# Optimization experiments

Measured on AMD Instinct MI355X. Metric: run time of the kernel, lower is better.

## Reference

```python
import jax, jax.numpy as jnp
import numpy as np
import math

DIM = 64
SCALE = math.sqrt(DIM)


def setup_inputs() -> dict:
    key = jax.random.key(0)
    k = jax.random.split(key, 6)
    B, N1, D, H, W = 4, 4096, DIM, 64, 64
    x = jax.random.normal(k[0], (B, N1, D), dtype=jnp.float32)
    y = jax.random.normal(k[1], (B, D, H, W), dtype=jnp.float32)
    # torch nn.Linear params: weight (out,in), bias (out,), uniform(-1/sqrt(in), 1/sqrt(in))
    bound = 1.0 / math.sqrt(D)
    w1 = jax.random.uniform(k[2], (D, D), jnp.float32, -bound, bound)
    b1 = jax.random.uniform(k[3], (D,), jnp.float32, -bound, bound)
    w2 = jax.random.uniform(k[4], (D, D), jnp.float32, -bound, bound)
    b2 = jax.random.uniform(k[5], (D,), jnp.float32, -bound, bound)
    return {"x": x, "y": y, "w1": w1, "b1": b1, "w2": w2, "b2": b2}


def reference(x, y, w1, b1, w2, b2):
    # x: (B, N1, D); y: (B, D, H, W)
    B, D, H, W = y.shape
    y_tok = jnp.transpose(y, (0, 2, 3, 1)).reshape(B, H * W, D)  # (B, N2, D)
    q1 = x @ w1.T + b1        # (B, N1, D)
    q2 = y_tok @ w2.T + b2    # (B, N2, D)
    attn = jnp.einsum('bnd,bmd->bnm', q1, q2) / SCALE  # (B, N1, N2)
    score = jax.nn.softmax(attn, axis=2)  # dropout is identity in eval
    # v1 = q1^T @ score, transposed -> (B, N2, D)
    v1 = jnp.einsum('bnd,bnm->bmd', q1, score)
    # v2 = q2^T @ score^T, transposed -> (B, N1, D)
    v2 = jnp.einsum('bmd,bnm->bnd', q2, score)
    v1_img = jnp.transpose(v1.reshape(B, H, W, D), (0, 3, 1, 2))  # (B, D, H, W)
    return (v2, v1_img)
```

## Files before the change

### kernel.cpp

```cpp
#include <hip/hip_runtime.h>
#include <hip/hip_bf16.h>


typedef __attribute__((ext_vector_type(8))) short s8v;
typedef __attribute__((ext_vector_type(4))) float f4v;
typedef unsigned short ushort_t;
typedef unsigned int uint_t;

constexpr int B = 4, N = 4096, D = 64, SPLIT = 8, MCH = N / SPLIT;
constexpr int CH = 64, NST = MCH / CH;
constexpr float C1 = 0.18033688011112042f;

#define MFMA(A, Bv, C) __builtin_amdgcn_mfma_f32_16x16x32_bf16(A, Bv, C, 0, 0, 0)

__device__ __forceinline__ ushort_t f2bf(float x) {
    __hip_bfloat16 h = __float2bfloat16(x);
    return *reinterpret_cast<ushort_t*>(&h);
}

__device__ __forceinline__ uint_t pk2(float lo, float hi) {
    __hip_bfloat162 h = __float22bfloat162_rn(make_float2(lo, hi));
    return *reinterpret_cast<uint_t*>(&h);
}

__device__ __forceinline__ float bf2f(ushort_t u) {
    return __uint_as_float(((uint_t)u) << 16);
}

__global__ __launch_bounds__(256) void k_proj_x(const float* __restrict__ x,
        const float* __restrict__ w, const float* __restrict__ bias,
        ushort_t* __restrict__ qb, ushort_t* __restrict__ qt) {
    __shared__ float Xs[64][68];
    __shared__ float Ws[64][68];
    __shared__ float Bs[64];
    const int b = blockIdx.y, n0 = blockIdx.x * 64, t = threadIdx.x;
    const float* xp = x + ((size_t)b * N + n0) * D;
    for (int j = t; j < 4096; j += 256) Xs[j >> 6][j & 63] = xp[j];
    for (int j = t; j < 4096; j += 256) Ws[j >> 6][j & 63] = w[j];
    if (t < 64) Bs[t] = bias[t];
    __syncthreads();
    const int d = t & 63, grp = t >> 6;
    float wr[64];
#pragma unroll
    for (int k4 = 0; k4 < 16; ++k4) {
        float4 v = *reinterpret_cast<const float4*>(&Ws[d][k4 * 4]);
        wr[4 * k4 + 0] = v.x; wr[4 * k4 + 1] = v.y;
        wr[4 * k4 + 2] = v.z; wr[4 * k4 + 3] = v.w;
    }
    for (int i = 0; i < 16; ++i) {
        const int r = grp * 16 + i;
        float acc = Bs[d];
#pragma unroll
        for (int k4 = 0; k4 < 16; ++k4) {
            float4 xv = *reinterpret_cast<const float4*>(&Xs[r][k4 * 4]);
            acc += xv.x * wr[4 * k4] + xv.y * wr[4 * k4 + 1] +
                   xv.z * wr[4 * k4 + 2] + xv.w * wr[4 * k4 + 3];
        }
        qb[((size_t)b * N + n0 + r) * D + d] = f2bf(acc);
        qt[((size_t)b * D + d) * N + n0 + r] = f2bf(acc);
    }
}

__global__ __launch_bounds__(256) void k_proj_y(const float* __restrict__ y,
        const float* __restrict__ w, const float* __restrict__ bias,
        ushort_t* __restrict__ qb, ushort_t* __restrict__ qt) {
    __shared__ float Ys[64][68];
    __shared__ float Ws[64][68];
    __shared__ float Bs[64];
    const int b = blockIdx.y, m0 = blockIdx.x * 64, t = threadIdx.x;
    const float* yp = y + (size_t)b * D * N;
    for (int j = t; j < 4096; j += 256) {
        int k = j >> 6, mm = j & 63;
        Ys[mm][k] = yp[(size_t)k * N + m0 + mm];
    }
    for (int j = t; j < 4096; j += 256) Ws[j >> 6][j & 63] = w[j];
    if (t < 64) Bs[t] = bias[t];
    __syncthreads();
    const int d = t & 63, grp = t >> 6;
    float wr[64];
#pragma unroll
    for (int k4 = 0; k4 < 16; ++k4) {
        float4 v = *reinterpret_cast<const float4*>(&Ws[d][k4 * 4]);
        wr[4 * k4 + 0] = v.x; wr[4 * k4 + 1] = v.y;
        wr[4 * k4 + 2] = v.z; wr[4 * k4 + 3] = v.w;
    }
    for (int i = 0; i < 16; ++i) {
        const int r = grp * 16 + i;
        float acc = Bs[d];
#pragma unroll
        for (int k4 = 0; k4 < 16; ++k4) {
            float4 xv = *reinterpret_cast<const float4*>(&Ys[r][k4 * 4]);
            acc += xv.x * wr[4 * k4] + xv.y * wr[4 * k4 + 1] +
                   xv.z * wr[4 * k4 + 2] + xv.w * wr[4 * k4 + 3];
        }
        qb[((size_t)b * N + m0 + r) * D + d] = f2bf(acc);
        qt[((size_t)b * D + d) * N + m0 + r] = f2bf(acc);
    }
}

template<bool WANT_SUM, bool OUT_DM>
__global__ __launch_bounds__(256, 4) void k_attn(
        const ushort_t* __restrict__ kbm,
        const ushort_t* __restrict__ qbm,
        const ushort_t* __restrict__ vtm,
        ushort_t* __restrict__ vout, float* __restrict__ ssump) {
    __shared__ ushort_t kbS[2][4096];
    __shared__ ushort_t ptS[4][2][512];
    const int b = blockIdx.z, sp = blockIdx.y;
    const int tid = threadIdx.x;
    const int w = tid >> 6, lane = tid & 63, g = lane >> 4, c = lane & 15;
    const int xs = (blockIdx.x & 7) * 4 + (blockIdx.x >> 3);
    const int wb = xs * 128 + w * 32;
    const int lo = sp * MCH;

    const int M = ((c >> 1) & 3) << 4;
    char* rowp0 = (char*)&ptS[w][0][0] + c * 64;
    char* rowp1 = (char*)&ptS[w][1][0] + c * 64;
    const int wo0 = (8 * g) ^ M, wo1 = (32 + 8 * g) ^ M;
    const int ro  = (16 * g) ^ M;

    const int swzc = (c & 7) << 4;

    s8v a[2][2];
#pragma unroll
    for (int rt = 0; rt < 2; ++rt) {
        const ushort_t* p = qbm + ((size_t)b * N + wb + rt * 16 + c) * D + 8 * g;
        a[rt][0] = *reinterpret_cast<const s8v*>(p);
        a[rt][1] = *reinterpret_cast<const s8v*>(p + 32);
    }

    const int s0 = tid * 16, s1 = s0 + 4096;
    const int p0 = s0 ^ (((s0 >> 7) & 7) << 4);
    const int p1 = s1 ^ (((s1 >> 7) & 7) << 4);
    const char* gkb = (const char*)(kbm + ((size_t)b * N + lo) * D);
    char* kb0 = (char*)&kbS[0][0];
    char* kb1 = (char*)&kbS[1][0];
    const ushort_t* vbase = vtm + ((size_t)b * D + c) * N + 8 * g;

    f4v accO[2][4] = {};
    float rs0 = 0.f, rs1 = 0.f;
    s8v kb[2][2], vt[4], pa0, pa1;

#define LDKB_LDS(KC, SUB)                                                     \
    {                                                                         \
        const char* _r0 = (KC) + (32 * (SUB) + c) * 128;                      \
        kb[0][0] = *reinterpret_cast<const s8v*>(_r0 + ((16 * g) ^ swzc));    \
        kb[0][1] = *reinterpret_cast<const s8v*>(_r0 + ((64 + 16 * g) ^ swzc)); \
        kb[1][0] = *reinterpret_cast<const s8v*>(_r0 + 2048 + ((16 * g) ^ swzc)); \
        kb[1][1] = *reinterpret_cast<const s8v*>(_r0 + 2048 + ((64 + 16 * g) ^ swzc)); \
    }
#define LDVT(P)                                                               \
    {                                                                         \
        _Pragma("unroll")                                                     \
        for (int dc = 0; dc < 4; ++dc)                                        \
            vt[dc] = *reinterpret_cast<const s8v*>(vbase + (size_t)dc * 16 * N + (P)); \
    }
#define QKEXP(PQ)                                                             \
    f4v PQ[2][2] = {};                                                        \
    __builtin_amdgcn_s_setprio(1);                                            \
    _Pragma("unroll")                                                         \
    for (int rt = 0; rt < 2; ++rt) {                                          \
        _Pragma("unroll")                                                     \
        for (int h = 0; h < 2; ++h) {                                         \
            PQ[rt][h] = MFMA(kb[h][0], a[rt][0], PQ[rt][h]);                  \
            PQ[rt][h] = MFMA(kb[h][1], a[rt][1], PQ[rt][h]);                  \
        }                                                                     \
    }                                                                         \
    __builtin_amdgcn_s_setprio(0);
#define PACKWRITE(PQ)                                                         \
    {                                                                         \
        _Pragma("unroll")                                                     \
        for (int rt = 0; rt < 2; ++rt) {                                      \
            char* rp = rt ? rowp1 : rowp0;                                    \
            float rsl = 0.f;                                                  \
            _Pragma("unroll")                                                 \
            for (int h = 0; h < 2; ++h) {                                     \
                float e0 = exp2f(PQ[rt][h][0] * C1);                          \
                float e1 = exp2f(PQ[rt][h][1] * C1);                          \
                float e2 = exp2f(PQ[rt][h][2] * C1);                          \
                float e3 = exp2f(PQ[rt][h][3] * C1);                          \
                if (WANT_SUM) rsl += (e0 + e1) + (e2 + e3);                   \
                uint2 pk = make_uint2(pk2(e0, e1), pk2(e2, e3));              \
                *reinterpret_cast<uint2*>(rp + (h ? wo1 : wo0)) = pk;         \
            }                                                                 \
            if (WANT_SUM) { if (rt) rs1 += rsl; else rs0 += rsl; }            \
        }                                                                     \
    }
#define PV()                                                                  \
    __builtin_amdgcn_s_setprio(1);                                            \
    _Pragma("unroll")                                                         \
    for (int dc = 0; dc < 4; ++dc) {                                          \
        accO[0][dc] = MFMA(pa0, vt[dc], accO[0][dc]);                         \
        accO[1][dc] = MFMA(pa1, vt[dc], accO[1][dc]);                         \
    }                                                                         \
    __builtin_amdgcn_s_setprio(0);
#define RDTILE()                                                              \
    pa0 = *reinterpret_cast<const s8v*>(rowp0 + ro);                          \
    pa1 = *reinterpret_cast<const s8v*>(rowp1 + ro);
#define SUBCHUNK(KC, SUB, M0)                                                 \
    {                                                                         \
        LDKB_LDS(KC, SUB)                                                     \
        QKEXP(pq)                                                             \
        PACKWRITE(pq)                                                         \
        LDVT(M0)                                                              \
        asm volatile("s_waitcnt lgkmcnt(0)" ::: "memory");                    \
        RDTILE()                                                              \
        PV()                                                                  \
    }

    {
        uint4 t0 = *reinterpret_cast<const uint4*>(gkb + s0);
        uint4 t1 = *reinterpret_cast<const uint4*>(gkb + s1);
        *reinterpret_cast<uint4*>(kb0 + p0) = t0;
        *reinterpret_cast<uint4*>(kb0 + p1) = t1;
    }
    __syncthreads();

    for (int i = 0; i < NST; ++i) {
        char* kcur = (i & 1) ? kb1 : kb0;
        char* knxt = (i & 1) ? kb0 : kb1;
        const char* gn = gkb + (((i + 1) & (NST - 1)) * (CH * D * 2));
        uint4 t0 = *reinterpret_cast<const uint4*>(gn + s0);
        uint4 t1 = *reinterpret_cast<const uint4*>(gn + s1);

        const int m0 = lo + i * CH;
        SUBCHUNK(kcur, 0, m0)
        SUBCHUNK(kcur, 1, m0 + 32)

        *reinterpret_cast<uint4*>(knxt + p0) = t0;
        *reinterpret_cast<uint4*>(knxt + p1) = t1;
        __syncthreads();
    }

#undef LDKB_LDS
#undef LDVT
#undef QKEXP
#undef PACKWRITE
#undef PV
#undef RDTILE
#undef SUBCHUNK

    const size_t ob = ((size_t)sp * B + b) * N;
    if (OUT_DM) {
#pragma unroll
        for (int rt = 0; rt < 2; ++rt)
#pragma unroll
            for (int dc = 0; dc < 4; ++dc) {
                size_t base = (((size_t)sp * B + b) * D + 16 * dc + c) * N
                              + wb + 16 * rt + 4 * g;
                uint2 pk = make_uint2(pk2(accO[rt][dc][0], accO[rt][dc][1]),
                                      pk2(accO[rt][dc][2], accO[rt][dc][3]));
                *reinterpret_cast<uint2*>(&vout[base]) = pk;
            }
    } else {
#pragma unroll
        for (int rt = 0; rt < 2; ++rt)
#pragma unroll
            for (int dc = 0; dc < 4; ++dc)
#pragma unroll
                for (int r = 0; r < 4; ++r)
                    vout[(ob + wb + 16 * rt + 4 * g + r) * D + 16 * dc + c] =
                        f2bf(accO[rt][dc][r]);
    }
    if (WANT_SUM) {
        rs0 += __shfl_xor(rs0, 16); rs0 += __shfl_xor(rs0, 32);
        rs1 += __shfl_xor(rs1, 16); rs1 += __shfl_xor(rs1, 32);
        if (g == 0) {
            ssump[ob + wb + c] = rs0;
            ssump[ob + wb + 16 + c] = rs1;
        }
    }
}

__global__ __launch_bounds__(256) void k_comb_v2(const ushort_t* __restrict__ v2p,
        const float* __restrict__ ssump, float* __restrict__ out,
        float* __restrict__ sinv) {
    const int t = blockIdx.x * 256 + threadIdx.x;
    const int bn = t >> 4, d0 = (t & 15) * 4;
    float S = 0.f;
#pragma unroll
    for (int s = 0; s < SPLIT; ++s) S += ssump[(size_t)s * B * N + bn];
    const float inv = 1.0f / S;
    f4v acc = {};
#pragma unroll
    for (int s = 0; s < SPLIT; ++s) {
        uint2 u = *reinterpret_cast<const uint2*>(
            &v2p[((size_t)s * B * N + bn) * D + d0]);
        acc[0] += bf2f((ushort_t)(u.x & 0xffff));
        acc[1] += bf2f((ushort_t)(u.x >> 16));
        acc[2] += bf2f((ushort_t)(u.y & 0xffff));
        acc[3] += bf2f((ushort_t)(u.y >> 16));
    }
    acc *= inv;
    *reinterpret_cast<f4v*>(&out[(size_t)bn * D + d0]) = acc;
    if (d0 == 0) sinv[bn] = inv;
}

__global__ __launch_bounds__(256) void k_scale(const ushort_t* __restrict__ q1t,
        const float* __restrict__ sinv, ushort_t* __restrict__ q1s) {
    const size_t t = ((size_t)blockIdx.x * 256 + threadIdx.x) * 8;
    const int b = (int)(t / ((size_t)D * N));
    const int n0 = (int)(t % N);
    s8v v = *reinterpret_cast<const s8v*>(q1t + t);
    const float* sv = sinv + (size_t)b * N + n0;
    s8v o;
#pragma unroll
    for (int j = 0; j < 8; ++j) {
        uint_t u = ((uint_t)(ushort_t)v[j]) << 16;
        float f = __uint_as_float(u) * sv[j];
        o[j] = (short)f2bf(f);
    }
    *reinterpret_cast<s8v*>(q1s + t) = o;
}

__global__ __launch_bounds__(256) void k_comb_v1(const ushort_t* __restrict__ v1p,
        float* __restrict__ out2) {
    const size_t t = ((size_t)blockIdx.x * 256 + threadIdx.x) * 4;
    f4v acc = {};
#pragma unroll
    for (int s = 0; s < SPLIT; ++s) {
        uint2 u = *reinterpret_cast<const uint2*>(&v1p[(size_t)s * B * D * N + t]);
        acc[0] += bf2f((ushort_t)(u.x & 0xffff));
        acc[1] += bf2f((ushort_t)(u.x >> 16));
        acc[2] += bf2f((ushort_t)(u.y & 0xffff));
        acc[3] += bf2f((ushort_t)(u.y >> 16));
    }
    *reinterpret_cast<f4v*>(&out2[t]) = acc;
}

extern "C" void kernel_launch(void* const* d_in, const int* in_sizes, int n_in,
                              void* d_out, int out_size, void* d_ws, size_t ws_size,
                              hipStream_t stream) {
    const float* x  = (const float*)d_in[0];
    const float* y  = (const float*)d_in[1];
    const float* w1 = (const float*)d_in[2];
    const float* b1 = (const float*)d_in[3];
    const float* w2 = (const float*)d_in[4];
    const float* b2 = (const float*)d_in[5];
    float* out = (float*)d_out;

    char* ws = (char*)d_ws;
    const size_t QE = (size_t)B * N * D;
    ushort_t* q1b = (ushort_t*)ws;
    ushort_t* q2b = q1b + QE;
    ushort_t* q1t = q2b + QE;
    ushort_t* q2t = q1t + QE;
    ushort_t* q1s = q2t + QE;
    float* fb   = (float*)(ws + QE * 5 * sizeof(ushort_t));
    float* sinv = fb;
    float* ssum = sinv + (size_t)B * N;
    ushort_t* vpart = (ushort_t*)(ssum + (size_t)SPLIT * B * N);

    dim3 blk(256);
    k_proj_x<<<dim3(N / 64, B), blk, 0, stream>>>(x, w1, b1, q1b, q1t);
    k_proj_y<<<dim3(N / 64, B), blk, 0, stream>>>(y, w2, b2, q2b, q2t);
    k_attn<true, false><<<dim3(N / 128, SPLIT, B), blk, 0, stream>>>(
        q2b, q1b, q2t, vpart, ssum);
    k_comb_v2<<<dim3(B * N * 16 / 256), blk, 0, stream>>>(vpart, ssum, out, sinv);
    k_scale<<<dim3((int)(QE / 8 / 256)), blk, 0, stream>>>(q1t, sinv, q1s);
    k_attn<false, true><<<dim3(N / 128, SPLIT, B), blk, 0, stream>>>(
        q1b, q2b, q1s, vpart, nullptr);
    k_comb_v1<<<dim3((int)(QE / 4 / 256)), blk, 0, stream>>>(vpart, out + QE);
}
```

Baseline: 116.5 us.

## Software-pipeline P·V MFMAs against next subchunk's QK and exp

```diff
diff --git a/kernel.cpp b/kernel.cpp
--- a/kernel.cpp
+++ b/kernel.cpp
@@ -105,7 +105,7 @@
         const ushort_t* __restrict__ vtm,
         ushort_t* __restrict__ vout, float* __restrict__ ssump) {
     __shared__ ushort_t kbS[2][4096];
-    __shared__ ushort_t ptS[4][2][512];
+    __shared__ ushort_t ptS[4][2][2][512];
     const int b = blockIdx.z, sp = blockIdx.y;
     const int tid = threadIdx.x;
     const int w = tid >> 6, lane = tid & 63, g = lane >> 4, c = lane & 15;
@@ -114,8 +114,7 @@
     const int lo = sp * MCH;
 
     const int M = ((c >> 1) & 3) << 4;
-    char* rowp0 = (char*)&ptS[w][0][0] + c * 64;
-    char* rowp1 = (char*)&ptS[w][1][0] + c * 64;
+    char* const pwc = (char*)&ptS[w][0][0][0] + c * 64;
     const int wo0 = (8 * g) ^ M, wo1 = (32 + 8 * g) ^ M;
     const int ro  = (16 * g) ^ M;
 
@@ -155,6 +154,9 @@
         for (int dc = 0; dc < 4; ++dc)                                        \
             vt[dc] = *reinterpret_cast<const s8v*>(vbase + (size_t)dc * 16 * N + (P)); \
     }
+#define RDP(SLOT)                                                             \
+    pa0 = *reinterpret_cast<const s8v*>(pwc + (SLOT) + ro);                   \
+    pa1 = *reinterpret_cast<const s8v*>(pwc + (SLOT) + 1024 + ro);
 #define QKEXP(PQ)                                                             \
     f4v PQ[2][2] = {};                                                        \
     __builtin_amdgcn_s_setprio(1);                                            \
@@ -167,11 +169,19 @@
         }                                                                     \
     }                                                                         \
     __builtin_amdgcn_s_setprio(0);
-#define PACKWRITE(PQ)                                                         \
+#define PVM()                                                                 \
+    __builtin_amdgcn_s_setprio(1);                                            \
+    _Pragma("unroll")                                                         \
+    for (int dc = 0; dc < 4; ++dc) {                                          \
+        accO[0][dc] = MFMA(pa0, vt[dc], accO[0][dc]);                         \
+        accO[1][dc] = MFMA(pa1, vt[dc], accO[1][dc]);                         \
+    }                                                                         \
+    __builtin_amdgcn_s_setprio(0);
+#define PACKWRITE(PQ, SLOT)                                                   \
     {                                                                         \
         _Pragma("unroll")                                                     \
         for (int rt = 0; rt < 2; ++rt) {                                      \
-            char* rp = rt ? rowp1 : rowp0;                                    \
+            char* rp = pwc + (SLOT) + rt * 1024;                              \
             float rsl = 0.f;                                                  \
             _Pragma("unroll")                                                 \
             for (int h = 0; h < 2; ++h) {                                     \
@@ -186,27 +196,6 @@
             if (WANT_SUM) { if (rt) rs1 += rsl; else rs0 += rsl; }            \
         }                                                                     \
     }
-#define PV()                                                                  \
-    __builtin_amdgcn_s_setprio(1);                                            \
-    _Pragma("unroll")                                                         \
-    for (int dc = 0; dc < 4; ++dc) {                                          \
-        accO[0][dc] = MFMA(pa0, vt[dc], accO[0][dc]);                         \
-        accO[1][dc] = MFMA(pa1, vt[dc], accO[1][dc]);                         \
-    }                                                                         \
-    __builtin_amdgcn_s_setprio(0);
-#define RDTILE()                                                              \
-    pa0 = *reinterpret_cast<const s8v*>(rowp0 + ro);                          \
-    pa1 = *reinterpret_cast<const s8v*>(rowp1 + ro);
-#define SUBCHUNK(KC, SUB, M0)                                                 \
-    {                                                                         \
-        LDKB_LDS(KC, SUB)                                                     \
-        QKEXP(pq)                                                             \
-        PACKWRITE(pq)                                                         \
-        LDVT(M0)                                                              \
-        asm volatile("s_waitcnt lgkmcnt(0)" ::: "memory");                    \
-        RDTILE()                                                              \
-        PV()                                                                  \
-    }
 
     {
         uint4 t0 = *reinterpret_cast<const uint4*>(gkb + s0);
@@ -216,7 +205,31 @@
     }
     __syncthreads();
 
-    for (int i = 0; i < NST; ++i) {
+    {
+        const char* gn = gkb + (CH * D * 2);
+        uint4 t0 = *reinterpret_cast<const uint4*>(gn + s0);
+        uint4 t1 = *reinterpret_cast<const uint4*>(gn + s1);
+
+        LDKB_LDS(kb0, 0)
+        {
+            QKEXP(pq0)
+            PACKWRITE(pq0, 0)
+            LDVT(lo)
+        }
+        RDP(0)
+        LDKB_LDS(kb0, 1)
+        {
+            QKEXP(pq1)
+            PVM()
+            PACKWRITE(pq1, 2048)
+            LDVT(lo + 32)
+        }
+        *reinterpret_cast<uint4*>(kb1 + p0) = t0;
+        *reinterpret_cast<uint4*>(kb1 + p1) = t1;
+        __syncthreads();
+    }
+
+    for (int i = 1; i < NST; ++i) {
         char* kcur = (i & 1) ? kb1 : kb0;
         char* knxt = (i & 1) ? kb0 : kb1;
         const char* gn = gkb + (((i + 1) & (NST - 1)) * (CH * D * 2));
@@ -224,21 +237,37 @@
         uint4 t1 = *reinterpret_cast<const uint4*>(gn + s1);
 
         const int m0 = lo + i * CH;
-        SUBCHUNK(kcur, 0, m0)
-        SUBCHUNK(kcur, 1, m0 + 32)
+        RDP(2048)
+        LDKB_LDS(kcur, 0)
+        {
+            QKEXP(pq0)
+            PVM()
+            PACKWRITE(pq0, 0)
+            LDVT(m0)
+        }
+        RDP(0)
+        LDKB_LDS(kcur, 1)
+        {
+            QKEXP(pq1)
+            PVM()
+            PACKWRITE(pq1, 2048)
+            LDVT(m0 + 32)
+        }
 
         *reinterpret_cast<uint4*>(knxt + p0) = t0;
         *reinterpret_cast<uint4*>(knxt + p1) = t1;
         __syncthreads();
     }
 
+    RDP(2048)
+    PVM()
+
 #undef LDKB_LDS
 #undef LDVT
+#undef RDP
 #undef QKEXP
+#undef PVM
 #undef PACKWRITE
-#undef PV
-#undef RDTILE
-#undef SUBCHUNK
 
     const size_t ob = ((size_t)sp * B + b) * N;
     if (OUT_DM) {
```

Result: slower. 153.8 us (+31.9%).

## Fold softmax normalization into exponent offset and batch both subchunks before PV

Applied to the files above, without the earlier changes.

```diff
diff --git a/kernel.cpp b/kernel.cpp
--- a/kernel.cpp
+++ b/kernel.cpp
@@ -98,14 +98,15 @@
     }
 }
 
-template<bool WANT_SUM, bool OUT_DM>
+template<bool WANT_SUM, bool OUT_DM, bool USE_OFF>
 __global__ __launch_bounds__(256, 4) void k_attn(
         const ushort_t* __restrict__ kbm,
         const ushort_t* __restrict__ qbm,
         const ushort_t* __restrict__ vtm,
+        const float* __restrict__ offl,
         ushort_t* __restrict__ vout, float* __restrict__ ssump) {
     __shared__ ushort_t kbS[2][4096];
-    __shared__ ushort_t ptS[4][2][512];
+    __shared__ ushort_t ptS[4][2048];
     const int b = blockIdx.z, sp = blockIdx.y;
     const int tid = threadIdx.x;
     const int w = tid >> 6, lane = tid & 63, g = lane >> 4, c = lane & 15;
@@ -114,8 +115,7 @@
     const int lo = sp * MCH;
 
     const int M = ((c >> 1) & 3) << 4;
-    char* rowp0 = (char*)&ptS[w][0][0] + c * 64;
-    char* rowp1 = (char*)&ptS[w][1][0] + c * 64;
+    char* const pwc = (char*)&ptS[w][0] + c * 64;
     const int wo0 = (8 * g) ^ M, wo1 = (32 + 8 * g) ^ M;
     const int ro  = (16 * g) ^ M;
 
@@ -136,10 +136,11 @@
     char* kb0 = (char*)&kbS[0][0];
     char* kb1 = (char*)&kbS[1][0];
     const ushort_t* vbase = vtm + ((size_t)b * D + c) * N + 8 * g;
+    const float* offb = USE_OFF ? (offl + (size_t)b * N + 4 * g) : nullptr;
 
     f4v accO[2][4] = {};
     float rs0 = 0.f, rs1 = 0.f;
-    s8v kb[2][2], vt[4], pa0, pa1;
+    s8v kb[2][2], vtA[4], vtB[4], paA0, paA1, paB0, paB1;
 
 #define LDKB_LDS(KC, SUB)                                                     \
     {                                                                         \
@@ -149,11 +150,11 @@
         kb[1][0] = *reinterpret_cast<const s8v*>(_r0 + 2048 + ((16 * g) ^ swzc)); \
         kb[1][1] = *reinterpret_cast<const s8v*>(_r0 + 2048 + ((64 + 16 * g) ^ swzc)); \
     }
-#define LDVT(P)                                                               \
+#define LDVT(ARR, P)                                                          \
     {                                                                         \
         _Pragma("unroll")                                                     \
         for (int dc = 0; dc < 4; ++dc)                                        \
-            vt[dc] = *reinterpret_cast<const s8v*>(vbase + (size_t)dc * 16 * N + (P)); \
+            (ARR)[dc] = *reinterpret_cast<const s8v*>(vbase + (size_t)dc * 16 * N + (P)); \
     }
 #define QKEXP(PQ)                                                             \
     f4v PQ[2][2] = {};                                                        \
@@ -167,18 +168,26 @@
         }                                                                     \
     }                                                                         \
     __builtin_amdgcn_s_setprio(0);
-#define PACKWRITE(PQ)                                                         \
+#define PACKWRITE(PQ, SLOT, M0)                                               \
     {                                                                         \
+        float lv0x = 0.f, lv0y = 0.f, lv0z = 0.f, lv0w = 0.f;                 \
+        float lv1x = 0.f, lv1y = 0.f, lv1z = 0.f, lv1w = 0.f;                 \
+        if (USE_OFF) {                                                        \
+            float4 l0 = *reinterpret_cast<const float4*>(offb + (M0));        \
+            float4 l1 = *reinterpret_cast<const float4*>(offb + (M0) + 16);   \
+            lv0x = l0.x; lv0y = l0.y; lv0z = l0.z; lv0w = l0.w;               \
+            lv1x = l1.x; lv1y = l1.y; lv1z = l1.z; lv1w = l1.w;               \
+        }                                                                     \
         _Pragma("unroll")                                                     \
         for (int rt = 0; rt < 2; ++rt) {                                      \
-            char* rp = rt ? rowp1 : rowp0;                                    \
+            char* rp = pwc + (SLOT) + rt * 1024;                              \
             float rsl = 0.f;                                                  \
             _Pragma("unroll")                                                 \
             for (int h = 0; h < 2; ++h) {                                     \
-                float e0 = exp2f(PQ[rt][h][0] * C1);                          \
-                float e1 = exp2f(PQ[rt][h][1] * C1);                          \
-                float e2 = exp2f(PQ[rt][h][2] * C1);                          \
-                float e3 = exp2f(PQ[rt][h][3] * C1);                          \
+                float e0 = exp2f(PQ[rt][h][0] * C1 + (h ? lv1x : lv0x));      \
+                float e1 = exp2f(PQ[rt][h][1] * C1 + (h ? lv1y : lv0y));      \
+                float e2 = exp2f(PQ[rt][h][2] * C1 + (h ? lv1z : lv0z));      \
+                float e3 = exp2f(PQ[rt][h][3] * C1 + (h ? lv1w : lv0w));      \
                 if (WANT_SUM) rsl += (e0 + e1) + (e2 + e3);                   \
                 uint2 pk = make_uint2(pk2(e0, e1), pk2(e2, e3));              \
                 *reinterpret_cast<uint2*>(rp + (h ? wo1 : wo0)) = pk;         \
@@ -186,27 +195,14 @@
             if (WANT_SUM) { if (rt) rs1 += rsl; else rs0 += rsl; }            \
         }                                                                     \
     }
-#define PV()                                                                  \
+#define PVM(PA0, PA1, VT)                                                     \
     __builtin_amdgcn_s_setprio(1);                                            \
     _Pragma("unroll")                                                         \
     for (int dc = 0; dc < 4; ++dc) {                                          \
-        accO[0][dc] = MFMA(pa0, vt[dc], accO[0][dc]);                         \
-        accO[1][dc] = MFMA(pa1, vt[dc], accO[1][dc]);                         \
+        accO[0][dc] = MFMA(PA0, (VT)[dc], accO[0][dc]);                       \
+        accO[1][dc] = MFMA(PA1, (VT)[dc], accO[1][dc]);                       \
     }                                                                         \
     __builtin_amdgcn_s_setprio(0);
-#define RDTILE()                                                              \
-    pa0 = *reinterpret_cast<const s8v*>(rowp0 + ro);                          \
-    pa1 = *reinterpret_cast<const s8v*>(rowp1 + ro);
-#define SUBCHUNK(KC, SUB, M0)                                                 \
-    {                                                                         \
-        LDKB_LDS(KC, SUB)                                                     \
-        QKEXP(pq)                                                             \
-        PACKWRITE(pq)                                                         \
-        LDVT(M0)                                                              \
-        asm volatile("s_waitcnt lgkmcnt(0)" ::: "memory");                    \
-        RDTILE()                                                              \
-        PV()                                                                  \
-    }
 
     {
         uint4 t0 = *reinterpret_cast<const uint4*>(gkb + s0);
@@ -224,8 +220,25 @@
         uint4 t1 = *reinterpret_cast<const uint4*>(gn + s1);
 
         const int m0 = lo + i * CH;
-        SUBCHUNK(kcur, 0, m0)
-        SUBCHUNK(kcur, 1, m0 + 32)
+        LDKB_LDS(kcur, 0)
+        {
+            QKEXP(pq0)
+            PACKWRITE(pq0, 0, lo + i * CH)
+        }
+        LDVT(vtA, m0)
+        LDKB_LDS(kcur, 1)
+        {
+            QKEXP(pq1)
+            PACKWRITE(pq1, 2048, lo + i * CH + 32)
+        }
+        LDVT(vtB, m0 + 32)
+        asm volatile("s_waitcnt lgkmcnt(0)" ::: "memory");
+        paA0 = *reinterpret_cast<const s8v*>(pwc + ro);
+        paA1 = *reinterpret_cast<const s8v*>(pwc + 1024 + ro);
+        paB0 = *reinterpret_cast<const s8v*>(pwc + 2048 + ro);
+        paB1 = *reinterpret_cast<const s8v*>(pwc + 3072 + ro);
+        PVM(paA0, paA1, vtA)
+        PVM(paB0, paB1, vtB)
 
         *reinterpret_cast<uint4*>(knxt + p0) = t0;
         *reinterpret_cast<uint4*>(knxt + p1) = t1;
@@ -236,9 +249,7 @@
 #undef LDVT
 #undef QKEXP
 #undef PACKWRITE
-#undef PV
-#undef RDTILE
-#undef SUBCHUNK
+#undef PVM
 
     const size_t ob = ((size_t)sp * B + b) * N;
     if (OUT_DM) {
@@ -274,7 +285,7 @@
 
 __global__ __launch_bounds__(256) void k_comb_v2(const ushort_t* __restrict__ v2p,
         const float* __restrict__ ssump, float* __restrict__ out,
-        float* __restrict__ sinv) {
+        float* __restrict__ offl) {
     const int t = blockIdx.x * 256 + threadIdx.x;
     const int bn = t >> 4, d0 = (t & 15) * 4;
     float S = 0.f;
@@ -293,24 +304,7 @@
     }
     acc *= inv;
     *reinterpret_cast<f4v*>(&out[(size_t)bn * D + d0]) = acc;
-    if (d0 == 0) sinv[bn] = inv;
-}
-
-__global__ __launch_bounds__(256) void k_scale(const ushort_t* __restrict__ q1t,
-        const float* __restrict__ sinv, ushort_t* __restrict__ q1s) {
-    const size_t t = ((size_t)blockIdx.x * 256 + threadIdx.x) * 8;
-    const int b = (int)(t / ((size_t)D * N));
-    const int n0 = (int)(t % N);
-    s8v v = *reinterpret_cast<const s8v*>(q1t + t);
-    const float* sv = sinv + (size_t)b * N + n0;
-    s8v o;
-#pragma unroll
-    for (int j = 0; j < 8; ++j) {
-        uint_t u = ((uint_t)(ushort_t)v[j]) << 16;
-        float f = __uint_as_float(u) * sv[j];
-        o[j] = (short)f2bf(f);
-    }
-    *reinterpret_cast<s8v*>(q1s + t) = o;
+    if (d0 == 0) offl[bn] = -__log2f(S);
 }
 
 __global__ __launch_bounds__(256) void k_comb_v1(const ushort_t* __restrict__ v1p,
@@ -345,20 +339,18 @@
     ushort_t* q2b = q1b + QE;
     ushort_t* q1t = q2b + QE;
     ushort_t* q2t = q1t + QE;
-    ushort_t* q1s = q2t + QE;
     float* fb   = (float*)(ws + QE * 5 * sizeof(ushort_t));
-    float* sinv = fb;
-    float* ssum = sinv + (size_t)B * N;
+    float* offl = fb;
+    float* ssum = offl + (size_t)B * N;
     ushort_t* vpart = (ushort_t*)(ssum + (size_t)SPLIT * B * N);
 
     dim3 blk(256);
     k_proj_x<<<dim3(N / 64, B), blk, 0, stream>>>(x, w1, b1, q1b, q1t);
     k_proj_y<<<dim3(N / 64, B), blk, 0, stream>>>(y, w2, b2, q2b, q2t);
-    k_attn<true, false><<<dim3(N / 128, SPLIT, B), blk, 0, stream>>>(
-        q2b, q1b, q2t, vpart, ssum);
-    k_comb_v2<<<dim3(B * N * 16 / 256), blk, 0, stream>>>(vpart, ssum, out, sinv);
-    k_scale<<<dim3((int)(QE / 8 / 256)), blk, 0, stream>>>(q1t, sinv, q1s);
-    k_attn<false, true><<<dim3(N / 128, SPLIT, B), blk, 0, stream>>>(
-        q1b, q2b, q1s, vpart, nullptr);
+    k_attn<true, false, false><<<dim3(N / 128, SPLIT, B), blk, 0, stream>>>(
+        q2b, q1b, q2t, nullptr, vpart, ssum);
+    k_comb_v2<<<dim3(B * N * 16 / 256), blk, 0, stream>>>(vpart, ssum, out, offl);
+    k_attn<false, true, true><<<dim3(N / 128, SPLIT, B), blk, 0, stream>>>(
+        q1b, q2b, q1t, offl, vpart, nullptr);
     k_comb_v1<<<dim3((int)(QE / 4 / 256)), blk, 0, stream>>>(vpart, out + QE);
 }
```

Result: slower. 136.6 us (+17.2%).
